# Optimization experiments

Hardware: AMD Instinct MI355X
Metric: run time of the kernel (lower is better)

The kernel has to match this reference:

```python
import jax, jax.numpy as jnp
import numpy as np

# Eigenvalue spec: (alpha, omega, multiplicity); field='complex' => d_state = sum(mul)
EIGS = [(-0.4, 0.0, 32), (-0.3, 3.14, 32), (-0.2, 6.28, 32), (-0.1, 12.57, 32),
        (-0.05, 25.13, 32), (-0.02, 50.27, 32), (-0.01, 100.53, 32), (-0.005, 201.06, 32)]
DELTA_MIN, DELTA_MAX = 1e-3, 1e-1
B_SZ, H, L = 8, 128, 8192  # batch, d_input, seq length


def setup_inputs() -> dict:
    key = jax.random.key(0)
    k_delta, k_bre, k_bim, k_cre, k_cim, k_d, k_u = jax.random.split(key, 7)
    # continuous-time diagonal state matrix Lambda (P,) complex
    Lam = np.concatenate([np.full(m, a + 1j * w, dtype=np.complex64) for a, w, m in EIGS])
    Lambda = jnp.asarray(Lam)  # (P,)
    P = Lambda.shape[0]
    # ZOH discretization (done at init in the torch module)
    Delta = DELTA_MIN + (DELTA_MAX - DELTA_MIN) * jax.random.uniform(k_delta, (P,), dtype=jnp.float32)
    Lambda_bar = jnp.exp(Lambda * Delta)  # (P,) complex64
    B = (jax.random.normal(k_bre, (P, H), dtype=jnp.float32)
         + 1j * jax.random.normal(k_bim, (P, H), dtype=jnp.float32))
    B_bar = (((Lambda_bar - 1.0) / Lambda)[:, None] * B).astype(jnp.complex64)  # (P,H)
    C_re = jax.random.normal(k_cre, (H, P), dtype=jnp.float32)
    C_im = jax.random.normal(k_cim, (H, P), dtype=jnp.float32)
    D = jax.random.normal(k_d, (H, H), dtype=jnp.float32)
    u = jax.random.normal(k_u, (B_SZ, H, L), dtype=jnp.float32)
    return {
        "u": u,
        "Lambda_bar_re": jnp.real(Lambda_bar), "Lambda_bar_im": jnp.imag(Lambda_bar),
        "B_bar_re": jnp.real(B_bar), "B_bar_im": jnp.imag(B_bar),
        "C_re": C_re, "C_im": C_im, "D": D,
    }


def reference(u, Lambda_bar_re, Lambda_bar_im, B_bar_re, B_bar_im, C_re, C_im, D):
    Lambda_bar = Lambda_bar_re + 1j * Lambda_bar_im          # (P,)
    B_bar = B_bar_re + 1j * B_bar_im                         # (P,H)
    C = C_re + 1j * C_im                                     # (H,P)
    uc = u.astype(B_bar.dtype)
    Bu = jnp.einsum('ph,bhl->bpl', B_bar, uc)                # (B,P,L) complex
    A = jnp.broadcast_to(Lambda_bar[None, :, None], Bu.shape)  # (B,P,L)
    # The repo's binary op computes the sequential recurrence x_t = A_t * (x_{t-1} + Bu_t).
    # Rewriting with Bu'_t = A_t * Bu_t gives x_t = A_t x_{t-1} + Bu'_t, which is the
    # standard (truly associative) first-order scan.
    ABu = A * Bu

    def binop(ei, ej):
        a_i, b_i = ei
        a_j, b_j = ej
        return a_j * a_i, a_j * b_i + b_j

    _, xs = jax.lax.associative_scan(binop, (A, ABu), axis=2)  # xs: (B,P,L)
    y = jnp.einsum('op,bpl->bol', C, xs).real + jnp.einsum('oh,bhl->bol', D, u)
    return jax.nn.gelu(y, approximate=False)  # torch nn.GELU default = exact erf
```

## Files before the change

### kernel.cpp

```cpp
#include <hip/hip_runtime.h>
#include <math.h>

#define Bn 8
#define Hd 128
#define Ld 8192
#define Pd 256
#define LC 32
#define NC 256

typedef __attribute__((ext_vector_type(8))) short bf16x8;
typedef __attribute__((ext_vector_type(4))) float f32x4;
#define MFMA16(a, b, c) __builtin_amdgcn_mfma_f32_16x16x32_bf16(a, b, c, 0, 0, 0)

__device__ __forceinline__ unsigned short f2bf(float f) {
  unsigned u = __float_as_uint(f);
  u = u + 0x7fffu + ((u >> 16) & 1u);
  return (unsigned short)(u >> 16);
}

#if __has_builtin(__builtin_amdgcn_cvt_pk_bf16_f32)
typedef __attribute__((ext_vector_type(2))) __bf16 v2bf_t;
__device__ __forceinline__ unsigned pack2(float a, float b) {
  v2bf_t r = __builtin_amdgcn_cvt_pk_bf16_f32(a, b);
  unsigned u;
  __builtin_memcpy(&u, &r, 4);
  return u;
}
#else
__device__ __forceinline__ unsigned pack2(float a, float b) {
  return (unsigned)f2bf(a) | ((unsigned)f2bf(b) << 16);
}
#endif

__device__ __forceinline__ float bflo(unsigned v) { return __uint_as_float(v << 16); }
__device__ __forceinline__ float bfhi(unsigned v) { return __uint_as_float(v & 0xffff0000u); }

__device__ __forceinline__ int bperm(int p) {
  return ((p & 4) << 2) | ((p & 16) >> 1) | ((p & 8) >> 1) | (p & 3);
}

__global__ void k_prep(const float* __restrict__ Bre, const float* __restrict__ Bim,
                       const float* __restrict__ Cre, const float* __restrict__ Cim,
                       const float* __restrict__ Dm,
                       bf16x8* __restrict__ Bfr, bf16x8* __restrict__ Bfi,
                       bf16x8* __restrict__ Cf, bf16x8* __restrict__ Df) {
  int tid = blockIdx.x * 256 + threadIdx.x;
  int lane = tid & 63, slot = tid >> 6;
  int q = lane >> 4, ln = lane & 15;
  if (slot < 64) {
    int ks = slot >> 4, mt = slot & 15;
    int p = mt * 16 + ln;
    bf16x8 vr, vi;
#pragma unroll
    for (int e = 0; e < 8; ++e) {
      int h = ks * 32 + q * 8 + e;
      vr[e] = (short)f2bf(Bre[p * Hd + h]);
      vi[e] = (short)f2bf(Bim[p * Hd + h]);
    }
    Bfr[slot * 64 + lane] = vr;
    Bfi[slot * 64 + lane] = vi;
  } else if (slot < 64 + 128) {
    int s2 = slot - 64;
    int ks = s2 >> 3, mt = s2 & 7;
    int o = mt * 16 + ln;
    bf16x8 v;
#pragma unroll
    for (int e = 0; e < 8; ++e) {
      int kp = ks * 32 + q * 8 + e;
      int p = kp >> 1;
      float val = (kp & 1) ? -Cim[o * Pd + p] : Cre[o * Pd + p];
      v[e] = (short)f2bf(val);
    }
    Cf[s2 * 64 + lane] = v;
  } else if (slot < 64 + 128 + 32) {
    int s3 = slot - 192;
    int ks = s3 >> 3, mt = s3 & 7;
    int o = mt * 16 + ln;
    bf16x8 v;
#pragma unroll
    for (int e = 0; e < 8; ++e) {
      int h = ks * 32 + q * 8 + e;
      v[e] = (short)f2bf(Dm[o * Hd + h]);
    }
    Df[s3 * 64 + lane] = v;
  }
}

__device__ __forceinline__ void stage_u(const float* __restrict__ ub, unsigned* us32, int t) {
  int lane = t & 63, w = t >> 6;
  int j0 = 4 * (lane & 7);
  int h2 = 16 * w + 2 * (lane >> 3);
  const float* r0 = ub + (size_t)h2 * Ld + j0;
  float4 a0 = *(const float4*)r0;
  float4 a1 = *(const float4*)(r0 + Ld);
  const float* r2 = r0 + (size_t)64 * Ld;
  float4 b0 = *(const float4*)r2;
  float4 b1 = *(const float4*)(r2 + Ld);
  float ta0[4] = {a0.x, a0.y, a0.z, a0.w};
  float ta1[4] = {a1.x, a1.y, a1.z, a1.w};
  float tb0[4] = {b0.x, b0.y, b0.z, b0.w};
  float tb1[4] = {b1.x, b1.y, b1.z, b1.w};
#pragma unroll
  for (int i = 0; i < 4; ++i) {
    int j = j0 + i;
    int g1 = (h2 >> 3) ^ (j & 7);
    us32[(j * 256 + (g1 << 4) + ((2 * h2) & 15)) >> 2] = pack2(ta0[i], ta1[i]);
    int hb = h2 + 64;
    int g2 = (hb >> 3) ^ (j & 7);
    us32[(j * 256 + (g2 << 4) + ((2 * hb) & 15)) >> 2] = pack2(tb0[i], tb1[i]);
  }
}

__device__ __forceinline__ void compute_bu(const unsigned* us32,
                                           const bf16x8* __restrict__ Bfr,
                                           const bf16x8* __restrict__ Bfi,
                                           unsigned* bu32, int t) {
  int lane = t & 63, w = t >> 6, q = lane >> 4, ln = lane & 15;
  f32x4 zz = {0.f, 0.f, 0.f, 0.f};
  f32x4 aR[4][2], aI[4][2];
#pragma unroll
  for (int mt = 0; mt < 4; ++mt)
#pragma unroll
    for (int n = 0; n < 2; ++n) { aR[mt][n] = zz; aI[mt][n] = zz; }

#pragma unroll
  for (int ks = 0; ks < 4; ++ks) {
    bf16x8 ubf[2];
#pragma unroll
    for (int n = 0; n < 2; ++n) {
      int j = 16 * n + ln;
      int g = (4 * ks + q) ^ (j & 7);
      ubf[n] = *(const bf16x8*)((const char*)us32 + j * 256 + g * 16);
    }
#pragma unroll
    for (int mt = 0; mt < 4; ++mt) {
      int tI = ks * 16 + w * 4 + mt;
      bf16x8 ar = Bfr[tI * 64 + lane];
      bf16x8 ai = Bfi[tI * 64 + lane];
#pragma unroll
      for (int n = 0; n < 2; ++n) {
        aR[mt][n] = MFMA16(ar, ubf[n], aR[mt][n]);
        aI[mt][n] = MFMA16(ai, ubf[n], aI[mt][n]);
      }
    }
  }
#pragma unroll
  for (int mt = 0; mt < 4; ++mt)
#pragma unroll
    for (int n = 0; n < 2; ++n)
#pragma unroll
      for (int r = 0; r < 4; ++r) {
        int p = w * 64 + mt * 16 + q * 4 + r;
        int j = 16 * n + ln;
        bu32[(p << 5) | (j ^ bperm(p))] = pack2(aR[mt][n][r], aI[mt][n][r]);
      }
}

__global__ __launch_bounds__(256, 4) void k_chunk(
    const float* __restrict__ u, const float* __restrict__ lre,
    const float* __restrict__ lim, const bf16x8* __restrict__ Bfr,
    const bf16x8* __restrict__ Bfi, float2* __restrict__ E,
    uint4* __restrict__ bu_g) {
  int bc = blockIdx.x;
  int b = bc >> 8, c = bc & 255;
  __shared__ __align__(16) unsigned char smem[8192 + 32768];
  unsigned* us32 = (unsigned*)smem;
  unsigned* bu32 = (unsigned*)(smem + 8192);
  int t = threadIdx.x;

  stage_u(u + (size_t)b * Hd * Ld + c * LC, us32, t);
  __syncthreads();
  compute_bu(us32, Bfr, Bfi, bu32, t);
  __syncthreads();

  int p = t;
  int pm = bperm(p);
  unsigned v[LC];
#pragma unroll
  for (int j = 0; j < LC; ++j) v[j] = bu32[(p << 5) | (j ^ pm)];

  float ax = lre[p], ay = lim[p];
  float xr = 0.f, xi = 0.f;
#pragma unroll
  for (int j = 0; j < LC; ++j) {
    float sr = xr + bflo(v[j]), si = xi + bfhi(v[j]);
    xr = ax * sr - ay * si;
    xi = ax * si + ay * sr;
  }
  E[(size_t)bc * Pd + p] = make_float2(xr, xi);
  uint4* dst = bu_g + ((size_t)bc * Pd + p) * 8;
#pragma unroll
  for (int i = 0; i < 8; ++i)
    dst[i] = make_uint4(v[4 * i + 0], v[4 * i + 1], v[4 * i + 2], v[4 * i + 3]);
}

__global__ __launch_bounds__(256) void k_scan(const float* __restrict__ lre,
                                              const float* __restrict__ lim,
                                              float2* __restrict__ E) {
  __shared__ float2 arr[32][8];
  int nb = blockIdx.x;
  int t = threadIdx.x;
  int pl = t & 7, rq = t >> 3;
  int b = nb >> 5;
  int p = ((nb & 31) << 3) + pl;
  float ax = lre[p], ay = lim[p];
  float mx = ax, my = ay;
#pragma unroll
  for (int k = 0; k < 5; ++k) {
    float nx = mx * mx - my * my, ny = 2.f * mx * my;
    mx = nx; my = ny;
  }
  size_t base = ((size_t)(b * NC + rq * 8)) * Pd + p;
  float2 pre[8];
  float cr = 0.f, ci = 0.f;
#pragma unroll
  for (int i = 0; i < 8; ++i) {
    float2 e = E[base + (size_t)i * Pd];
    pre[i] = make_float2(cr, ci);
    float nx = mx * cr - my * ci + e.x;
    float ny = mx * ci + my * cr + e.y;
    cr = nx; ci = ny;
  }
  float Mx = mx, My = my;
#pragma unroll
  for (int k = 0; k < 3; ++k) {
    float nx = Mx * Mx - My * My, ny = 2.f * Mx * My;
    Mx = nx; My = ny;
  }
  float Vx = cr, Vy = ci;
#pragma unroll
  for (int d = 1; d < 32; d <<= 1) {
    arr[rq][pl] = make_float2(Vx, Vy);
    __syncthreads();
    if (rq >= d) {
      float2 pv = arr[rq - d][pl];
      Vx += Mx * pv.x - My * pv.y;
      Vy += Mx * pv.y + My * pv.x;
    }
    __syncthreads();
    float nx = Mx * Mx - My * My, ny = 2.f * Mx * My;
    Mx = nx; My = ny;
  }
  arr[rq][pl] = make_float2(Vx, Vy);
  __syncthreads();
  float Cx = 0.f, Cy = 0.f;
  if (rq > 0) {
    float2 pv = arr[rq - 1][pl];
    Cx = pv.x; Cy = pv.y;
  }
  float tx = 1.f, ty = 0.f;
#pragma unroll
  for (int i = 0; i < 8; ++i) {
    float ox = pre[i].x + tx * Cx - ty * Cy;
    float oy = pre[i].y + tx * Cy + ty * Cx;
    E[base + (size_t)i * Pd] = make_float2(ox, oy);
    float nx = tx * mx - ty * my, ny = tx * my + ty * mx;
    tx = nx; ty = ny;
  }
}

__global__ __launch_bounds__(256, 4) void k_main(
    const float* __restrict__ u, const float* __restrict__ lre,
    const float* __restrict__ lim, const bf16x8* __restrict__ Cf,
    const bf16x8* __restrict__ Df, const float2* __restrict__ E,
    const uint4* __restrict__ bu_g, float* __restrict__ out) {
  int bc = blockIdx.x;
  int b = bc >> 8, c = bc & 255;
  __shared__ __align__(16) unsigned char smem[8192 + 32768];
  unsigned* us32 = (unsigned*)smem;
  unsigned* xs32 = (unsigned*)(smem + 8192);
  int t = threadIdx.x;
  int lane = t & 63, w = t >> 6, q = lane >> 4, ln = lane & 15;

  stage_u(u + (size_t)b * Hd * Ld + c * LC, us32, t);

  int p = t;
  const uint4* src = bu_g + ((size_t)bc * Pd + p) * 8;
  uint4 bv[8];
#pragma unroll
  for (int i = 0; i < 8; ++i) bv[i] = src[i];
  float2 xin = E[(size_t)bc * Pd + p];
  {
    float ax = lre[p], ay = lim[p];
    float xr = xin.x, xi = xin.y;
#pragma unroll
    for (int i = 0; i < 8; ++i) {
      unsigned ww[4] = {bv[i].x, bv[i].y, bv[i].z, bv[i].w};
#pragma unroll
      for (int e = 0; e < 4; ++e) {
        int j = 4 * i + e;
        unsigned vj = ww[e];
        float sr = xr + bflo(vj), si = xi + bfhi(vj);
        xr = ax * sr - ay * si;
        xi = ax * si + ay * sr;
        xs32[j * 256 + ((((p >> 2) ^ (j & 7)) << 2) + (p & 3))] = pack2(xr, xi);
      }
    }
  }
  __syncthreads();

  f32x4 zz = {0.f, 0.f, 0.f, 0.f};
  f32x4 acc[2][2] = {{zz, zz}, {zz, zz}};
#pragma unroll
  for (int ks = 0; ks < 16; ++ks) {
    bf16x8 xb[2];
#pragma unroll
    for (int n = 0; n < 2; ++n) {
      int j = 16 * n + ln;
      int g = (4 * ks + q) ^ (j & 7);
      xb[n] = *(const bf16x8*)((const char*)xs32 + j * 1024 + g * 16);
    }
#pragma unroll
    for (int mt = 0; mt < 2; ++mt) {
      bf16x8 cf = Cf[(ks * 8 + w * 2 + mt) * 64 + lane];
#pragma unroll
      for (int n = 0; n < 2; ++n) acc[mt][n] = MFMA16(cf, xb[n], acc[mt][n]);
    }
  }
#pragma unroll
  for (int ks = 0; ks < 4; ++ks) {
    bf16x8 ubf[2];
#pragma unroll
    for (int n = 0; n < 2; ++n) {
      int j = 16 * n + ln;
      int g = (4 * ks + q) ^ (j & 7);
      ubf[n] = *(const bf16x8*)((const char*)us32 + j * 256 + g * 16);
    }
#pragma unroll
    for (int mt = 0; mt < 2; ++mt) {
      bf16x8 df = Df[(ks * 8 + w * 2 + mt) * 64 + lane];
#pragma unroll
      for (int n = 0; n < 2; ++n) acc[mt][n] = MFMA16(df, ubf[n], acc[mt][n]);
    }
  }

#pragma unroll
  for (int mt = 0; mt < 2; ++mt)
#pragma unroll
    for (int n = 0; n < 2; ++n)
#pragma unroll
      for (int r = 0; r < 4; ++r) {
        int o = w * 32 + mt * 16 + q * 4 + r;
        int l = c * LC + 16 * n + ln;
        float vy = acc[mt][n][r];
        float e2 = __builtin_amdgcn_exp2f(-2.4554670f * vy);
        float gy = vy * __builtin_amdgcn_rcpf(1.0f + e2);
        out[((size_t)(b * Hd + o)) * Ld + l] = gy;
      }
}

extern "C" void kernel_launch(void* const* d_in, const int* in_sizes, int n_in,
                              void* d_out, int out_size, void* d_ws, size_t ws_size,
                              hipStream_t stream) {
  const float* u   = (const float*)d_in[0];
  const float* lre = (const float*)d_in[1];
  const float* lim = (const float*)d_in[2];
  const float* Bre = (const float*)d_in[3];
  const float* Bim = (const float*)d_in[4];
  const float* Cre = (const float*)d_in[5];
  const float* Cim = (const float*)d_in[6];
  const float* Dm  = (const float*)d_in[7];
  float* out = (float*)d_out;

  char* ws = (char*)d_ws;
  bf16x8* Bfr = (bf16x8*)(ws);
  bf16x8* Bfi = (bf16x8*)(ws + 65536);
  bf16x8* Cf  = (bf16x8*)(ws + 131072);
  bf16x8* Df  = (bf16x8*)(ws + 262144);
  float2* E   = (float2*)(ws + (1 << 20));
  uint4*  buw = (uint4*)(ws + (8u << 20));

  k_prep<<<56, 256, 0, stream>>>(Bre, Bim, Cre, Cim, Dm, Bfr, Bfi, Cf, Df);
  k_chunk<<<Bn * NC, 256, 0, stream>>>(u, lre, lim, Bfr, Bfi, E, buw);
  k_scan<<<256, 256, 0, stream>>>(lre, lim, E);
  k_main<<<Bn * NC, 256, 0, stream>>>(u, lre, lim, Cf, Df, E, (const uint4*)buw, out);
}
```

Baseline: 163.3 us.

## Recompute Bu in main kernel instead of storing it to global memory

The chunk kernel no longer writes the Bu intermediate to a global workspace; it only computes chunk-end states. The main kernel restages u, recomputes Bu via MFMA into shared memory, reads it into registers, then reuses the same shared buffer for the state sequence. This removes a large global write and read of the intermediate at the cost of repeating the Bu GEMM and adding barriers.

After: 147.5 us. 9.7% less time.

```diff
diff --git a/kernel.cpp b/kernel.cpp
--- a/kernel.cpp
+++ b/kernel.cpp
@@ -159,8 +159,7 @@
 __global__ __launch_bounds__(256, 4) void k_chunk(
     const float* __restrict__ u, const float* __restrict__ lre,
     const float* __restrict__ lim, const bf16x8* __restrict__ Bfr,
-    const bf16x8* __restrict__ Bfi, float2* __restrict__ E,
-    uint4* __restrict__ bu_g) {
+    const bf16x8* __restrict__ Bfi, float2* __restrict__ E) {
   int bc = blockIdx.x;
   int b = bc >> 8, c = bc & 255;
   __shared__ __align__(16) unsigned char smem[8192 + 32768];
@@ -175,23 +174,16 @@
 
   int p = t;
   int pm = bperm(p);
-  unsigned v[LC];
-#pragma unroll
-  for (int j = 0; j < LC; ++j) v[j] = bu32[(p << 5) | (j ^ pm)];
-
   float ax = lre[p], ay = lim[p];
   float xr = 0.f, xi = 0.f;
 #pragma unroll
   for (int j = 0; j < LC; ++j) {
-    float sr = xr + bflo(v[j]), si = xi + bfhi(v[j]);
+    unsigned v = bu32[(p << 5) | (j ^ pm)];
+    float sr = xr + bflo(v), si = xi + bfhi(v);
     xr = ax * sr - ay * si;
     xi = ax * si + ay * sr;
   }
   E[(size_t)bc * Pd + p] = make_float2(xr, xi);
-  uint4* dst = bu_g + ((size_t)bc * Pd + p) * 8;
-#pragma unroll
-  for (int i = 0; i < 8; ++i)
-    dst[i] = make_uint4(v[4 * i + 0], v[4 * i + 1], v[4 * i + 2], v[4 * i + 3]);
 }
 
 __global__ __launch_bounds__(256) void k_scan(const float* __restrict__ lre,
@@ -261,40 +253,41 @@
 
 __global__ __launch_bounds__(256, 4) void k_main(
     const float* __restrict__ u, const float* __restrict__ lre,
-    const float* __restrict__ lim, const bf16x8* __restrict__ Cf,
+    const float* __restrict__ lim, const bf16x8* __restrict__ Bfr,
+    const bf16x8* __restrict__ Bfi, const bf16x8* __restrict__ Cf,
     const bf16x8* __restrict__ Df, const float2* __restrict__ E,
-    const uint4* __restrict__ bu_g, float* __restrict__ out) {
+    float* __restrict__ out) {
   int bc = blockIdx.x;
   int b = bc >> 8, c = bc & 255;
   __shared__ __align__(16) unsigned char smem[8192 + 32768];
   unsigned* us32 = (unsigned*)smem;
-  unsigned* xs32 = (unsigned*)(smem + 8192);
+  unsigned* bu32 = (unsigned*)(smem + 8192);
+  unsigned* xs32 = bu32;
   int t = threadIdx.x;
   int lane = t & 63, w = t >> 6, q = lane >> 4, ln = lane & 15;
 
   stage_u(u + (size_t)b * Hd * Ld + c * LC, us32, t);
+  __syncthreads();
+  compute_bu(us32, Bfr, Bfi, bu32, t);
+  __syncthreads();
 
   int p = t;
-  const uint4* src = bu_g + ((size_t)bc * Pd + p) * 8;
-  uint4 bv[8];
-#pragma unroll
-  for (int i = 0; i < 8; ++i) bv[i] = src[i];
+  int pm = bperm(p);
+  unsigned v[LC];
+#pragma unroll
+  for (int j = 0; j < LC; ++j) v[j] = bu32[(p << 5) | (j ^ pm)];
   float2 xin = E[(size_t)bc * Pd + p];
+  __syncthreads();
+
   {
     float ax = lre[p], ay = lim[p];
     float xr = xin.x, xi = xin.y;
 #pragma unroll
-    for (int i = 0; i < 8; ++i) {
-      unsigned ww[4] = {bv[i].x, bv[i].y, bv[i].z, bv[i].w};
-#pragma unroll
-      for (int e = 0; e < 4; ++e) {
-        int j = 4 * i + e;
-        unsigned vj = ww[e];
-        float sr = xr + bflo(vj), si = xi + bfhi(vj);
-        xr = ax * sr - ay * si;
-        xi = ax * si + ay * sr;
-        xs32[j * 256 + ((((p >> 2) ^ (j & 7)) << 2) + (p & 3))] = pack2(xr, xi);
-      }
+    for (int j = 0; j < LC; ++j) {
+      float sr = xr + bflo(v[j]), si = xi + bfhi(v[j]);
+      xr = ax * sr - ay * si;
+      xi = ax * si + ay * sr;
+      xs32[j * 256 + ((((p >> 2) ^ (j & 7)) << 2) + (p & 3))] = pack2(xr, xi);
     }
   }
   __syncthreads();
@@ -368,10 +361,9 @@
   bf16x8* Cf  = (bf16x8*)(ws + 131072);
   bf16x8* Df  = (bf16x8*)(ws + 262144);
   float2* E   = (float2*)(ws + (1 << 20));
-  uint4*  buw = (uint4*)(ws + (8u << 20));
 
   k_prep<<<56, 256, 0, stream>>>(Bre, Bim, Cre, Cim, Dm, Bfr, Bfi, Cf, Df);
-  k_chunk<<<Bn * NC, 256, 0, stream>>>(u, lre, lim, Bfr, Bfi, E, buw);
+  k_chunk<<<Bn * NC, 256, 0, stream>>>(u, lre, lim, Bfr, Bfi, E);
   k_scan<<<256, 256, 0, stream>>>(lre, lim, E);
-  k_main<<<Bn * NC, 256, 0, stream>>>(u, lre, lim, Cf, Df, E, (const uint4*)buw, out);
-}
+  k_main<<<Bn * NC, 256, 0, stream>>>(u, lre, lim, Bfr, Bfi, Cf, Df, E, out);
+}
```
